# Performance work log

Hardware: AMD Instinct MI355X
Metric: run time of the kernel (lower is better)

Reference implementation:

```python
import jax, jax.numpy as jnp
import numpy as np

N = 50000      # nodes
E = 800000     # edges
IN = 128       # in_feats
HID = 16       # h_feats (per head)
HEADS = 8      # num_heads layer 1
CLS = 40       # num_classes
NEG_SLOPE = 0.2


def setup_inputs() -> dict:
    key = jax.random.key(0)
    ks = jax.random.split(key, 12)
    s = lambda fan: np.float32(1.0 / np.sqrt(fan))
    return {
        "features": jax.random.normal(ks[0], (N, IN), jnp.float32),
        "edge_src": jax.random.randint(ks[1], (E,), 0, N, dtype=jnp.int32),
        "edge_dst": jax.random.randint(ks[2], (E,), 0, N, dtype=jnp.int32),
        # layer 1 params
        "W1": jax.random.normal(ks[3], (IN, HEADS * HID), jnp.float32) * s(IN),
        "al1": jax.random.normal(ks[4], (HEADS, HID), jnp.float32) * s(HID),
        "ar1": jax.random.normal(ks[5], (HEADS, HID), jnp.float32) * s(HID),
        "b1": jnp.zeros((HEADS * HID,), jnp.float32),
        # layer 2 params (1 head)
        "W2": jax.random.normal(ks[6], (HEADS * HID, CLS), jnp.float32) * s(HEADS * HID),
        "al2": jax.random.normal(ks[7], (1, CLS), jnp.float32) * s(CLS),
        "ar2": jax.random.normal(ks[8], (1, CLS), jnp.float32) * s(CLS),
        "b2": jnp.zeros((CLS,), jnp.float32),
    }


def gat_conv(x, W, al, ar, b, src, dst, heads, out_dim):
    # x: [N, F_in] -> feat: [N, H, D]
    feat = (x @ W).reshape(-1, heads, out_dim)
    el = (feat * al).sum(-1)                      # [N, H]
    er = (feat * ar).sum(-1)                      # [N, H]
    e = jax.nn.leaky_relu(el[src] + er[dst], NEG_SLOPE)  # [E, H]
    # segment softmax over destination neighborhoods
    emax = jax.ops.segment_max(e, dst, num_segments=N)   # [N, H]
    emax = jnp.where(jnp.isfinite(emax), emax, jnp.float32(0.0))
    ee = jnp.exp(e - emax[dst])                   # [E, H]
    denom = jax.ops.segment_sum(ee, dst, num_segments=N)
    alpha = ee / (denom[dst] + jnp.float32(1e-9)) # [E, H]
    msg = alpha[:, :, None] * feat[src]           # [E, H, D]
    out = jax.ops.segment_sum(msg, dst, num_segments=N)  # [N, H, D]
    return out + b.reshape(1, heads, out_dim)


def reference(features, edge_src, edge_dst, W1, al1, ar1, b1, W2, al2, ar2, b2):
    h = jax.nn.elu(gat_conv(features, W1, al1, ar1, b1, edge_src, edge_dst, HEADS, HID))
    h = h.reshape(N, HEADS * HID)                 # flatten(1)
    out = gat_conv(h, W2, al2, ar2, b2, edge_src, edge_dst, 1, CLS)
    return out.mean(axis=1)                       # [N, CLS]
```

## Files before the change

kernel.cpp:

```cpp
#include <hip/hip_runtime.h>
#include <hip/hip_bf16.h>

#define N_NODES 50000
#define N_EDGES 800000
#define IN_F    128
#define HID     16
#define HEADS   8
#define F1      128
#define CLS     40
#define CLSP    64
#define NEG     0.2f
#define SLOT    64

#define GEMM1_BLOCKS ((N_NODES + 63) / 64)
#define SCAT_BLOCKS  ((N_EDGES + 255) / 256)

typedef __bf16 bf16x8 __attribute__((ext_vector_type(8)));
typedef float  f32x4  __attribute__((ext_vector_type(4)));
typedef float  f32x2  __attribute__((ext_vector_type(2)));

__device__ __forceinline__ float leaky(float v) { return v >= 0.0f ? v : NEG * v; }
__device__ __forceinline__ f32x2 unpk(unsigned u) {
    f32x2 r;
    r.x = __uint_as_float(u << 16);
    r.y = __uint_as_float(u & 0xffff0000u);
    return r;
}

__global__ void setup_kernel(const float* __restrict__ W1, const float* __restrict__ W2,
                             __bf16* __restrict__ w1t, __bf16* __restrict__ w2t,
                             int* __restrict__ cursor) {
    int i = blockIdx.x * blockDim.x + threadIdx.x;
    if (i < N_NODES) cursor[i] = 0;
    if (i < 128 * 128) {
        int n = i >> 7, k = i & 127;
        w1t[i] = (__bf16)W1[k * 128 + n];
    }
    if (i < CLSP * 128) {
        int n = i >> 7, k = i & 127;
        w2t[i] = (n < CLS) ? (__bf16)W2[k * CLS + n] : (__bf16)0.0f;
    }
}

__device__ __forceinline__ void gemm1_body(int bid, int tid,
                                           const float* __restrict__ A,
                                           const __bf16* __restrict__ Wt,
                                           const float* __restrict__ al1,
                                           const float* __restrict__ ar1,
                                           __bf16* __restrict__ outb,
                                           float* __restrict__ el,
                                           float* __restrict__ er) {
    int wave = tid >> 6, lane = tid & 63;
    int m0 = bid * 64 + wave * 16;
    int c = lane & 15;
    int row = m0 + c;
    int rowc = row < N_NODES ? row : N_NODES - 1;
    int ko = (lane >> 4) * 8;

    f32x4 acc[8];
    #pragma unroll
    for (int t = 0; t < 8; ++t)
        #pragma unroll
        for (int r = 0; r < 4; ++r) acc[t][r] = 0.f;

    for (int ks = 0; ks < 128; ks += 32) {
        const float* ap = A + (size_t)rowc * 128 + ks + ko;
        float4 u = *(const float4*)ap;
        float4 v = *(const float4*)(ap + 4);
        bf16x8 a;
        a[0] = (__bf16)u.x; a[1] = (__bf16)u.y; a[2] = (__bf16)u.z; a[3] = (__bf16)u.w;
        a[4] = (__bf16)v.x; a[5] = (__bf16)v.y; a[6] = (__bf16)v.z; a[7] = (__bf16)v.w;
        #pragma unroll
        for (int t = 0; t < 8; ++t) {
            bf16x8 b = *(const bf16x8*)(Wt + (size_t)(t * 16 + c) * 128 + ks + ko);
            acc[t] = __builtin_amdgcn_mfma_f32_16x16x32_bf16(a, b, acc[t], 0, 0, 0);
        }
    }
    int rbase = m0 + (lane >> 4) * 4;
    #pragma unroll
    for (int t = 0; t < 8; ++t) {
        int gcol = t * 16 + c;
        #pragma unroll
        for (int r = 0; r < 4; ++r) {
            int grow = rbase + r;
            if (grow < N_NODES) outb[(size_t)grow * 128 + gcol] = (__bf16)acc[t][r];
        }
    }
    #pragma unroll
    for (int t = 0; t < 8; ++t) {
        float alv = al1[t * 16 + c];
        float arv = ar1[t * 16 + c];
        float pe[4], pr[4];
        #pragma unroll
        for (int r = 0; r < 4; ++r) { pe[r] = acc[t][r] * alv; pr[r] = acc[t][r] * arv; }
        #pragma unroll
        for (int mask = 1; mask <= 8; mask <<= 1) {
            #pragma unroll
            for (int r = 0; r < 4; ++r) {
                pe[r] += __shfl_xor(pe[r], mask, 64);
                pr[r] += __shfl_xor(pr[r], mask, 64);
            }
        }
        if (c == 0) {
            #pragma unroll
            for (int r = 0; r < 4; ++r) {
                int grow = rbase + r;
                if (grow < N_NODES) {
                    el[grow * 8 + t] = pe[r];
                    er[grow * 8 + t] = pr[r];
                }
            }
        }
    }
}

__device__ __forceinline__ void scatter_body(int bid, int tid,
                                             const int* __restrict__ src,
                                             const int* __restrict__ dst,
                                             int* __restrict__ cursor,
                                             unsigned short* __restrict__ srcs16) {
    int e = bid * 256 + tid;
    if (e >= N_EDGES) return;
    int d = dst[e];
    int c = atomicAdd(&cursor[d], 1);
    if (c < SLOT) srcs16[d * SLOT + c] = (unsigned short)src[e];
}

__global__ __launch_bounds__(256) void fat_gemm1_scatter(const float* __restrict__ A,
                                                         const __bf16* __restrict__ Wt,
                                                         const float* __restrict__ al1,
                                                         const float* __restrict__ ar1,
                                                         __bf16* __restrict__ outb,
                                                         float* __restrict__ el,
                                                         float* __restrict__ er,
                                                         const int* __restrict__ esrc,
                                                         const int* __restrict__ edst,
                                                         int* __restrict__ cursor,
                                                         unsigned short* __restrict__ srcs16) {
    if (blockIdx.x < GEMM1_BLOCKS)
        gemm1_body(blockIdx.x, threadIdx.x, A, Wt, al1, ar1, outb, el, er);
    else
        scatter_body(blockIdx.x - GEMM1_BLOCKS, threadIdx.x, esrc, edst, cursor, srcs16);
}

__global__ __launch_bounds__(256) void gemm2_mfma(const __bf16* __restrict__ A,
                                                  const __bf16* __restrict__ Wt,
                                                  const float* __restrict__ al2,
                                                  const float* __restrict__ ar2,
                                                  __bf16* __restrict__ out,
                                                  float* __restrict__ el,
                                                  float* __restrict__ er) {
    int wave = threadIdx.x >> 6, lane = threadIdx.x & 63;
    int m0 = blockIdx.x * 64 + wave * 16;
    int c = lane & 15;
    int row = m0 + c;
    int rowc = row < N_NODES ? row : N_NODES - 1;
    int ko = (lane >> 4) * 8;

    f32x4 acc[3];
    #pragma unroll
    for (int t = 0; t < 3; ++t)
        #pragma unroll
        for (int r = 0; r < 4; ++r) acc[t][r] = 0.f;

    for (int ks = 0; ks < 128; ks += 32) {
        bf16x8 a = *(const bf16x8*)(A + (size_t)rowc * 128 + ks + ko);
        #pragma unroll
        for (int t = 0; t < 3; ++t) {
            bf16x8 b = *(const bf16x8*)(Wt + (size_t)(t * 16 + c) * 128 + ks + ko);
            acc[t] = __builtin_amdgcn_mfma_f32_16x16x32_bf16(a, b, acc[t], 0, 0, 0);
        }
    }
    int rbase = m0 + (lane >> 4) * 4;
    #pragma unroll
    for (int t = 0; t < 3; ++t) {
        int gcol = t * 16 + c;
        #pragma unroll
        for (int r = 0; r < 4; ++r) {
            int grow = rbase + r;
            if (grow < N_NODES && gcol < CLS)
                out[(size_t)grow * CLS + gcol] = (__bf16)acc[t][r];
        }
    }
    float pe[4] = {0.f, 0.f, 0.f, 0.f}, pr[4] = {0.f, 0.f, 0.f, 0.f};
    #pragma unroll
    for (int t = 0; t < 3; ++t) {
        int idx = t * 16 + c;
        float alv = (idx < CLS) ? al2[idx] : 0.f;
        float arv = (idx < CLS) ? ar2[idx] : 0.f;
        #pragma unroll
        for (int r = 0; r < 4; ++r) { pe[r] += acc[t][r] * alv; pr[r] += acc[t][r] * arv; }
    }
    #pragma unroll
    for (int mask = 1; mask <= 8; mask <<= 1) {
        #pragma unroll
        for (int r = 0; r < 4; ++r) {
            pe[r] += __shfl_xor(pe[r], mask, 64);
            pr[r] += __shfl_xor(pr[r], mask, 64);
        }
    }
    if (c == 0) {
        #pragma unroll
        for (int r = 0; r < 4; ++r) {
            int grow = rbase + r;
            if (grow < N_NODES) { el[grow] = pe[r]; er[grow] = pr[r]; }
        }
    }
}

__global__ __launch_bounds__(256) void gat1_fused(const int* __restrict__ degs,
                                                  const unsigned short* __restrict__ srcs,
                                                  const float* __restrict__ el,
                                                  const float* __restrict__ er,
                                                  const __bf16* __restrict__ feat1b,
                                                  const float* __restrict__ b1,
                                                  __bf16* __restrict__ hbufb) {
    int wave = threadIdx.x >> 6;
    int lane = threadIdx.x & 63;
    int d = blockIdx.x * 4 + wave;
    int off = d * SLOT;
    int deg = min(degs[d], SLOT);

    int q = lane >> 4, fg = lane & 15, hd = fg >> 1;
    float er_d = er[d * 8 + hd];

    f32x2 accv[4];
    #pragma unroll
    for (int j = 0; j < 4; ++j) { accv[j].x = 0.f; accv[j].y = 0.f; }
    float dsum = 0.f;

    int ng = (deg + 3) >> 2;
    #pragma unroll 4
    for (int g = 0; g < ng; ++g) {
        int k = g * 4 + q;
        bool ok = k < deg;
        int s = ok ? (int)srcs[off + k] : 0;
        float elv = el[s * 8 + hd];
        uint4 p = *(const uint4*)(feat1b + (size_t)s * F1 + fg * 8);
        float w = ok ? __expf(leaky(elv + er_d)) : 0.f;
        dsum += w;
        f32x2 av; av.x = w; av.y = w;
        accv[0] += av * unpk(p.x);
        accv[1] += av * unpk(p.y);
        accv[2] += av * unpk(p.z);
        accv[3] += av * unpk(p.w);
    }

    float acc[8];
    #pragma unroll
    for (int j = 0; j < 4; ++j) { acc[2 * j] = accv[j].x; acc[2 * j + 1] = accv[j].y; }
    #pragma unroll
    for (int i = 0; i < 8; ++i) {
        acc[i] += __shfl_xor(acc[i], 16, 64);
        acc[i] += __shfl_xor(acc[i], 32, 64);
    }
    dsum += __shfl_xor(dsum, 16, 64);
    dsum += __shfl_xor(dsum, 32, 64);
    float inv_l = 1.f / (dsum + 1e-9f);

    if (q == 0) {
        bf16x8 o;
        #pragma unroll
        for (int i = 0; i < 8; ++i) {
            float v = acc[i] * inv_l + b1[fg * 8 + i];
            v = v > 0.f ? v : expm1f(v);
            o[i] = (__bf16)v;
        }
        *(bf16x8*)(hbufb + (size_t)d * F1 + fg * 8) = o;
    }
}

__global__ __launch_bounds__(256) void gat2_fused(const int* __restrict__ degs,
                                                  const unsigned short* __restrict__ srcs,
                                                  const float* __restrict__ el,
                                                  const float* __restrict__ er,
                                                  const __bf16* __restrict__ feat2p,
                                                  const float* __restrict__ b2,
                                                  float* __restrict__ out) {
    int wave = threadIdx.x >> 6;
    int lane = threadIdx.x & 63;
    int d = blockIdx.x * 4 + wave;
    int off = d * SLOT;
    int deg = min(degs[d], SLOT);

    float er_d = er[d];
    int q  = lane >> 4;
    int cg = lane & 15;
    f32x2 accv[2];
    accv[0].x = 0.f; accv[0].y = 0.f; accv[1].x = 0.f; accv[1].y = 0.f;
    float dsum = 0.f;

    int ng = (deg + 3) >> 2;
    #pragma unroll 4
    for (int g = 0; g < ng; ++g) {
        int k = g * 4 + q;
        bool ok = k < deg;
        int s = ok ? (int)srcs[off + k] : 0;
        float elv = el[s];
        uint2 p;
        p.x = 0u; p.y = 0u;
        if (cg < 10) p = *(const uint2*)(feat2p + (size_t)s * CLS + cg * 4);
        float w = ok ? __expf(leaky(elv + er_d)) : 0.f;
        dsum += w;
        f32x2 av; av.x = w; av.y = w;
        accv[0] += av * unpk(p.x);
        accv[1] += av * unpk(p.y);
    }

    float acc[4];
    acc[0] = accv[0].x; acc[1] = accv[0].y; acc[2] = accv[1].x; acc[3] = accv[1].y;
    #pragma unroll
    for (int i = 0; i < 4; ++i) {
        acc[i] += __shfl_xor(acc[i], 16, 64);
        acc[i] += __shfl_xor(acc[i], 32, 64);
    }
    dsum += __shfl_xor(dsum, 16, 64);
    dsum += __shfl_xor(dsum, 32, 64);
    float inv_l = 1.f / (dsum + 1e-9f);

    if (lane < 10) {
        float4 o;
        o.x = acc[0] * inv_l + b2[cg * 4 + 0];
        o.y = acc[1] * inv_l + b2[cg * 4 + 1];
        o.z = acc[2] * inv_l + b2[cg * 4 + 2];
        o.w = acc[3] * inv_l + b2[cg * 4 + 3];
        *(float4*)(out + (size_t)d * CLS + cg * 4) = o;
    }
}

extern "C" void kernel_launch(void* const* d_in, const int* in_sizes, int n_in,
                              void* d_out, int out_size, void* d_ws, size_t ws_size,
                              hipStream_t stream) {
    const float* features = (const float*)d_in[0];
    const int*   esrc     = (const int*)d_in[1];
    const int*   edst     = (const int*)d_in[2];
    const float* W1       = (const float*)d_in[3];
    const float* al1      = (const float*)d_in[4];
    const float* ar1      = (const float*)d_in[5];
    const float* b1       = (const float*)d_in[6];
    const float* W2       = (const float*)d_in[7];
    const float* al2      = (const float*)d_in[8];
    const float* ar2      = (const float*)d_in[9];
    const float* b2       = (const float*)d_in[10];
    float* out = (float*)d_out;

    float* ws = (float*)d_ws;
    float*          el1    = ws;
    float*          er1    = ws + 400000;
    float*          el2    = ws + 800000;
    float*          er2    = ws + 850000;
    int*            cursor = (int*)(ws + 900000);
    unsigned short* srcs16 = (unsigned short*)(ws + 950000);
    __bf16*         feat1b = (__bf16*)(ws + 2550000);
    __bf16*         hbufb  = (__bf16*)(ws + 5750000);
    __bf16*         feat2p = (__bf16*)(ws + 8950000);
    __bf16*         w1t    = (__bf16*)(ws + 9950000);
    __bf16*         w2t    = (__bf16*)(ws + 9958192);

    const int B = 256;

    setup_kernel<<<(N_NODES + B - 1) / B, B, 0, stream>>>(W1, W2, w1t, w2t, cursor);

    fat_gemm1_scatter<<<GEMM1_BLOCKS + SCAT_BLOCKS, B, 0, stream>>>(
        features, w1t, al1, ar1, feat1b, el1, er1, esrc, edst, cursor, srcs16);

    gat1_fused<<<N_NODES / 4, B, 0, stream>>>(cursor, srcs16, el1, er1, feat1b, b1, hbufb);

    gemm2_mfma<<<(N_NODES + 63) / 64, B, 0, stream>>>(hbufb, w2t, al2, ar2,
                                                      feat2p, el2, er2);

    gat2_fused<<<N_NODES / 4, B, 0, stream>>>(cursor, srcs16, el2, er2, feat2p, b2, out);
}
```

Before: 239.4 us.

## Split layer-1 features into per-head-pair planes for cache-friendly gathers

The GEMM1 output features and attention logits are stored as four planes, each holding two heads (32 columns), instead of one row-major 128-wide array. The layer-1 aggregation kernel now handles one plane per block, with a 16-lane group per destination node and four edges processed in parallel. Each plane is 3.2MB, so its gather working set is smaller and more likely to stay in cache. GEMM2 reads the planar hidden buffer. In exchange, source indices and degrees are read four times and exp is computed redundantly per lane.

```diff
diff --git a/kernel.cpp b/kernel.cpp
--- a/kernel.cpp
+++ b/kernel.cpp
@@ -14,6 +14,8 @@
 
 #define GEMM1_BLOCKS ((N_NODES + 63) / 64)
 #define SCAT_BLOCKS  ((N_EDGES + 255) / 256)
+#define PLANE32 ((size_t)N_NODES * 32)
+#define PLANE2  ((size_t)N_NODES * 2)
 
 typedef __bf16 bf16x8 __attribute__((ext_vector_type(8)));
 typedef float  f32x4  __attribute__((ext_vector_type(4)));
@@ -47,9 +49,9 @@
                                            const __bf16* __restrict__ Wt,
                                            const float* __restrict__ al1,
                                            const float* __restrict__ ar1,
-                                           __bf16* __restrict__ outb,
-                                           float* __restrict__ el,
-                                           float* __restrict__ er) {
+                                           __bf16* __restrict__ featp,
+                                           float* __restrict__ elp,
+                                           float* __restrict__ erp) {
     int wave = tid >> 6, lane = tid & 63;
     int m0 = bid * 64 + wave * 16;
     int c = lane & 15;
@@ -79,11 +81,12 @@
     int rbase = m0 + (lane >> 4) * 4;
     #pragma unroll
     for (int t = 0; t < 8; ++t) {
-        int gcol = t * 16 + c;
+        int hp = t >> 1, cp = (t & 1) * 16 + c;
         #pragma unroll
         for (int r = 0; r < 4; ++r) {
             int grow = rbase + r;
-            if (grow < N_NODES) outb[(size_t)grow * 128 + gcol] = (__bf16)acc[t][r];
+            if (grow < N_NODES)
+                featp[(size_t)hp * PLANE32 + (size_t)grow * 32 + cp] = (__bf16)acc[t][r];
         }
     }
     #pragma unroll
@@ -106,8 +109,8 @@
             for (int r = 0; r < 4; ++r) {
                 int grow = rbase + r;
                 if (grow < N_NODES) {
-                    el[grow * 8 + t] = pe[r];
-                    er[grow * 8 + t] = pr[r];
+                    elp[(size_t)(t >> 1) * PLANE2 + grow * 2 + (t & 1)] = pe[r];
+                    erp[(size_t)(t >> 1) * PLANE2 + grow * 2 + (t & 1)] = pr[r];
                 }
             }
         }
@@ -130,20 +133,88 @@
                                                          const __bf16* __restrict__ Wt,
                                                          const float* __restrict__ al1,
                                                          const float* __restrict__ ar1,
-                                                         __bf16* __restrict__ outb,
-                                                         float* __restrict__ el,
-                                                         float* __restrict__ er,
+                                                         __bf16* __restrict__ featp,
+                                                         float* __restrict__ elp,
+                                                         float* __restrict__ erp,
                                                          const int* __restrict__ esrc,
                                                          const int* __restrict__ edst,
                                                          int* __restrict__ cursor,
                                                          unsigned short* __restrict__ srcs16) {
     if (blockIdx.x < GEMM1_BLOCKS)
-        gemm1_body(blockIdx.x, threadIdx.x, A, Wt, al1, ar1, outb, el, er);
+        gemm1_body(blockIdx.x, threadIdx.x, A, Wt, al1, ar1, featp, elp, erp);
     else
         scatter_body(blockIdx.x - GEMM1_BLOCKS, threadIdx.x, esrc, edst, cursor, srcs16);
 }
 
-__global__ __launch_bounds__(256) void gemm2_mfma(const __bf16* __restrict__ A,
+__global__ __launch_bounds__(256) void gat1_sliced(const int* __restrict__ degs,
+                                                   const unsigned short* __restrict__ srcs,
+                                                   const float* __restrict__ elp,
+                                                   const float* __restrict__ erp,
+                                                   const __bf16* __restrict__ featp,
+                                                   const float* __restrict__ b1,
+                                                   __bf16* __restrict__ hbufp) {
+    int hp = blockIdx.x & 3;
+    int chunk = blockIdx.x >> 2;
+    int wave = threadIdx.x >> 6, lane = threadIdx.x & 63;
+    int g2 = lane >> 4;
+    int e4 = (lane >> 2) & 3;
+    int L  = lane & 3;
+    int d = chunk * 16 + wave * 4 + g2;
+    int off = d * SLOT;
+    int deg = min(degs[d], SLOT);
+
+    const float*  elh = elp + (size_t)hp * PLANE2;
+    const __bf16* fpl = featp + (size_t)hp * PLANE32;
+    f32x2 erd = *(const f32x2*)(erp + (size_t)hp * PLANE2 + d * 2);
+
+    f32x2 accv[4];
+    #pragma unroll
+    for (int j = 0; j < 4; ++j) { accv[j].x = 0.f; accv[j].y = 0.f; }
+    float dsum = 0.f;
+
+    int ng = (deg + 3) >> 2;
+    #pragma unroll 4
+    for (int g = 0; g < ng; ++g) {
+        int e = g * 4 + e4;
+        bool ok = e < deg;
+        int s = ok ? (int)srcs[off + e] : 0;
+        f32x2 elv = *(const f32x2*)(elh + s * 2);
+        uint4 p = *(const uint4*)(fpl + (size_t)s * 32 + L * 8);
+        float w0 = __expf(leaky(elv.x + erd.x));
+        float w1 = __expf(leaky(elv.y + erd.y));
+        float w = (L < 2) ? w0 : w1;
+        w = ok ? w : 0.f;
+        dsum += w;
+        f32x2 av; av.x = w; av.y = w;
+        accv[0] += av * unpk(p.x);
+        accv[1] += av * unpk(p.y);
+        accv[2] += av * unpk(p.z);
+        accv[3] += av * unpk(p.w);
+    }
+
+    float acc[8];
+    #pragma unroll
+    for (int j = 0; j < 4; ++j) { acc[2 * j] = accv[j].x; acc[2 * j + 1] = accv[j].y; }
+    #pragma unroll
+    for (int i = 0; i < 8; ++i) {
+        acc[i] += __shfl_xor(acc[i], 4, 64);
+        acc[i] += __shfl_xor(acc[i], 8, 64);
+    }
+    dsum += __shfl_xor(dsum, 4, 64);
+    dsum += __shfl_xor(dsum, 8, 64);
+    float inv_l = 1.f / (dsum + 1e-9f);
+
+    bf16x8 o;
+    #pragma unroll
+    for (int i = 0; i < 8; ++i) {
+        float v = acc[i] * inv_l + b1[hp * 32 + L * 8 + i];
+        v = v > 0.f ? v : expm1f(v);
+        o[i] = (__bf16)v;
+    }
+    *(bf16x8*)(hbufp + (size_t)hp * PLANE32 + (size_t)d * 32 + L * 8) = o;
+}
+
+__global__ __launch_bounds__(256) void gemm2_mfma(const __bf16* __restrict__ Ap,
                                                   const __bf16* __restrict__ Wt,
                                                   const float* __restrict__ al2,
                                                   const float* __restrict__ ar2,
@@ -164,7 +235,9 @@
         for (int r = 0; r < 4; ++r) acc[t][r] = 0.f;
 
     for (int ks = 0; ks < 128; ks += 32) {
-        bf16x8 a = *(const bf16x8*)(A + (size_t)rowc * 128 + ks + ko);
+        int f = ks + ko;
+        bf16x8 a = *(const bf16x8*)(Ap + (size_t)(f >> 5) * PLANE32
+                                       + (size_t)rowc * 32 + (f & 31));
         #pragma unroll
         for (int t = 0; t < 3; ++t) {
             bf16x8 b = *(const bf16x8*)(Wt + (size_t)(t * 16 + c) * 128 + ks + ko);
@@ -205,68 +278,6 @@
             int grow = rbase + r;
             if (grow < N_NODES) { el[grow] = pe[r]; er[grow] = pr[r]; }
         }
-    }
-}
-
-__global__ __launch_bounds__(256) void gat1_fused(const int* __restrict__ degs,
-                                                  const unsigned short* __restrict__ srcs,
-                                                  const float* __restrict__ el,
-                                                  const float* __restrict__ er,
-                                                  const __bf16* __restrict__ feat1b,
-                                                  const float* __restrict__ b1,
-                                                  __bf16* __restrict__ hbufb) {
-    int wave = threadIdx.x >> 6;
-    int lane = threadIdx.x & 63;
-    int d = blockIdx.x * 4 + wave;
-    int off = d * SLOT;
-    int deg = min(degs[d], SLOT);
-
-    int q = lane >> 4, fg = lane & 15, hd = fg >> 1;
-    float er_d = er[d * 8 + hd];
-
-    f32x2 accv[4];
-    #pragma unroll
-    for (int j = 0; j < 4; ++j) { accv[j].x = 0.f; accv[j].y = 0.f; }
-    float dsum = 0.f;
-
-    int ng = (deg + 3) >> 2;
-    #pragma unroll 4
-    for (int g = 0; g < ng; ++g) {
-        int k = g * 4 + q;
-        bool ok = k < deg;
-        int s = ok ? (int)srcs[off + k] : 0;
-        float elv = el[s * 8 + hd];
-        uint4 p = *(const uint4*)(feat1b + (size_t)s * F1 + fg * 8);
-        float w = ok ? __expf(leaky(elv + er_d)) : 0.f;
-        dsum += w;
-        f32x2 av; av.x = w; av.y = w;
-        accv[0] += av * unpk(p.x);
-        accv[1] += av * unpk(p.y);
-        accv[2] += av * unpk(p.z);
-        accv[3] += av * unpk(p.w);
-    }
-
-    float acc[8];
-    #pragma unroll
-    for (int j = 0; j < 4; ++j) { acc[2 * j] = accv[j].x; acc[2 * j + 1] = accv[j].y; }
-    #pragma unroll
-    for (int i = 0; i < 8; ++i) {
-        acc[i] += __shfl_xor(acc[i], 16, 64);
-        acc[i] += __shfl_xor(acc[i], 32, 64);
-    }
-    dsum += __shfl_xor(dsum, 16, 64);
-    dsum += __shfl_xor(dsum, 32, 64);
-    float inv_l = 1.f / (dsum + 1e-9f);
-
-    if (q == 0) {
-        bf16x8 o;
-        #pragma unroll
-        for (int i = 0; i < 8; ++i) {
-            float v = acc[i] * inv_l + b1[fg * 8 + i];
-            v = v > 0.f ? v : expm1f(v);
-            o[i] = (__bf16)v;
-        }
-        *(bf16x8*)(hbufb + (size_t)d * F1 + fg * 8) = o;
     }
 }
 
@@ -345,14 +356,14 @@
     float* out = (float*)d_out;
 
     float* ws = (float*)d_ws;
-    float*          el1    = ws;
-    float*          er1    = ws + 400000;
+    float*          elp    = ws;
+    float*          erp    = ws + 400000;
     float*          el2    = ws + 800000;
     float*          er2    = ws + 850000;
     int*            cursor = (int*)(ws + 900000);
     unsigned short* srcs16 = (unsigned short*)(ws + 950000);
-    __bf16*         feat1b = (__bf16*)(ws + 2550000);
-    __bf16*         hbufb  = (__bf16*)(ws + 5750000);
+    __bf16*         featp  = (__bf16*)(ws + 2550000);
+    __bf16*         hbufp  = (__bf16*)(ws + 5750000);
     __bf16*         feat2p = (__bf16*)(ws + 8950000);
     __bf16*         w1t    = (__bf16*)(ws + 9950000);
     __bf16*         w2t    = (__bf16*)(ws + 9958192);
@@ -362,11 +373,12 @@
     setup_kernel<<<(N_NODES + B - 1) / B, B, 0, stream>>>(W1, W2, w1t, w2t, cursor);
 
     fat_gemm1_scatter<<<GEMM1_BLOCKS + SCAT_BLOCKS, B, 0, stream>>>(
-        features, w1t, al1, ar1, feat1b, el1, er1, esrc, edst, cursor, srcs16);
-
-    gat1_fused<<<N_NODES / 4, B, 0, stream>>>(cursor, srcs16, el1, er1, feat1b, b1, hbufb);
-
-    gemm2_mfma<<<(N_NODES + 63) / 64, B, 0, stream>>>(hbufb, w2t, al2, ar2,
+        features, w1t, al1, ar1, featp, elp, erp, esrc, edst, cursor, srcs16);
+
+    gat1_sliced<<<(N_NODES / 16) * 4, B, 0, stream>>>(cursor, srcs16, elp, erp,
+                                                      featp, b1, hbufp);
+
+    gemm2_mfma<<<(N_NODES + 63) / 64, B, 0, stream>>>(hbufp, w2t, al2, ar2,
                                                       feat2p, el2, er2);
 
     gat2_fused<<<N_NODES / 4, B, 0, stream>>>(cursor, srcs16, el2, er2, feat2p, b2, out);
```

Result: no change. 238.8 us (-0.3%).
